# Kernel tuning notes

Measured on AMD Instinct MI355X. Metric: run time of the kernel, lower is better.

The kernel has to match this reference:

```python
import jax, jax.numpy as jnp
import numpy as np

PATCH = 3  # patch_size=3, stride=1
B, C, H, W = 8, 256, 64, 64


def _extract_patches(x):
    # x: (c, h, w) -> (c*PATCH*PATCH, N) with N = (h-2)*(w-2), valid 3x3 patches
    c, h, w = x.shape
    hh, ww = h - PATCH + 1, w - PATCH + 1
    pats = jnp.stack([x[:, i:i + hh, j:j + ww]
                      for i in range(PATCH) for j in range(PATCH)], axis=0)  # (9, c, hh, ww)
    return pats.reshape(PATCH * PATCH * c, hh * ww)


def _index_to_flow(max_idx):
    # max_idx: (hh, ww) int -> flow (h, w, 2) padded by 2 at bottom/right
    hh, ww = max_idx.shape
    flow_w = (max_idx % ww).astype(jnp.float32)
    flow_h = (max_idx // ww).astype(jnp.float32)
    gy, gx = jnp.meshgrid(jnp.arange(hh, dtype=jnp.float32),
                          jnp.arange(ww, dtype=jnp.float32), indexing='ij')
    flow = jnp.stack((flow_w - gx, flow_h - gy), axis=2)  # (hh, ww, 2)
    return jnp.pad(flow, ((0, 2), (0, 2), (0, 0)))


def _per_image(feat_in, feat_ref):
    c, h, w = feat_in.shape
    hh, ww = h - PATCH + 1, w - PATCH + 1
    # channel-wise L2 normalize each spatial position (F.normalize dim=0, eps=1e-12)
    feat_in = feat_in / jnp.maximum(jnp.linalg.norm(feat_in, axis=0, keepdims=True), 1e-12)
    feat_ref = feat_ref / jnp.maximum(jnp.linalg.norm(feat_ref, axis=0, keepdims=True), 1e-12)
    Pi = _extract_patches(feat_in)    # (k, N)
    Pr = _extract_patches(feat_ref)   # (k, N)
    # is_norm=True: normalize ref patches (norm + 1e-5, per BasicSR feature_match_index)
    Pr = Pr / (jnp.linalg.norm(Pr, axis=0, keepdims=True) + 1e-5)
    corr = Pi.T @ Pr                  # (N, N) exhaustive patch correlation
    max_val = corr.max(axis=1)
    max_idx = jnp.argmax(corr, axis=1)
    # norm_input=True: divide by input patch norms
    max_val = max_val / jnp.linalg.norm(Pi, axis=0)
    max_val = max_val.reshape(hh, ww)
    max_idx = max_idx.reshape(hh, ww)
    sim = jnp.pad(max_val, ((1, 1), (1, 1)))[None]  # (1, h, w)
    flow = _index_to_flow(max_idx)                   # (h, w, 2)
    # nine down-right shifts (fill 0 at top-left), tensor_shift semantics
    shifted = jnp.stack([jnp.pad(flow[:h - i, :w - j], ((i, 0), (j, 0), (0, 0)))
                         for i in range(3) for j in range(3)], axis=0)  # (9, h, w, 2)
    return flow, shifted, sim


def setup_inputs() -> dict:
    key = jax.random.key(0)
    k1, k2 = jax.random.split(key)
    features1 = jax.random.normal(k1, (B, C, H, W), dtype=jnp.float32)
    features2 = jax.random.normal(k2, (B, C, H, W), dtype=jnp.float32)
    return {"features1": features1, "features2": features2}


def reference(features1, features2):
    pre_flow, pre_offset, pre_similarity = jax.vmap(_per_image)(features1, features2)
    # pre_flow: (b,h,w,2); pre_offset: (b,9,h,w,2); pre_similarity: (b,1,h,w)
    return pre_flow, pre_offset, pre_similarity
```

## Files before the change

### kernel.cpp

```cpp
#include <hip/hip_runtime.h>

typedef unsigned short u16;
typedef unsigned char u8;
typedef unsigned int u32;
typedef __bf16 bf16x8 __attribute__((ext_vector_type(8)));
typedef float f32x4 __attribute__((ext_vector_type(4)));

constexpr int BATCH = 8;
constexpr int C = 256;
constexpr int H = 64;
constexpr int W = 64;
constexpr int HW = H * W;
constexpr int HH = 62, WW = 62;
constexpr int NQ = HH * WW;
constexpr int SEG = 8;
constexpr int NBLK_RED = 536;

constexpr size_t OFF_RNORM = 0;
constexpr size_t OFF_RESV = 262144;
constexpr size_t OFF_RESI = 385280;
constexpr size_t OFF_PV = 508416;
constexpr size_t OFF_PI = OFF_PV + 62980096;
constexpr size_t OFF_SLOT0 = OFF_PI + 15745024;
constexpr size_t SP_H1 = 0;
constexpr size_t SP_L1 = 2097152;
constexpr size_t SP_H2 = 4194304;
constexpr size_t SP_L2 = 6291456;
constexpr size_t SP_Q = 8388608;
constexpr size_t SLOT_BYTES = 75513856;
constexpr size_t PVIMG = (size_t)NQ * 512;

typedef const __attribute__((address_space(1))) unsigned int* gas_ptr;
typedef __attribute__((address_space(3))) unsigned int* las_ptr;
__device__ __forceinline__ void gl16(const void* g, void* l) {
  __builtin_amdgcn_global_load_lds((gas_ptr)g, (las_ptr)l, 16, 0, 0);
}

__device__ __forceinline__ int pre_of(int ki) {
  if (ki <= 62) return ki * (ki + 1) / 2;
  int r = 123 - ki;
  return 1953 + 1891 - r * (r + 1) / 2;
}

__global__ __launch_bounds__(256) void norm_kernel(const float* __restrict__ f1,
                                                   const float* __restrict__ f2,
                                                   float* __restrict__ rnorm) {
  int by = blockIdx.x;
  int tensor = blockIdx.y;
  const float* f = tensor ? f2 : f1;
  int b = by >> 6, y = by & 63;
  int x = threadIdx.x & 63;
  int cq = threadIdx.x >> 6;
  const float* base = f + ((size_t)b * C) * HW + y * W + x;
  float s = 0.f;
  for (int c = cq; c < C; c += 4) {
    float v = base[(size_t)c * HW];
    s = fmaf(v, v, s);
  }
  __shared__ float sm[4][64];
  sm[cq][x] = s;
  __syncthreads();
  if (threadIdx.x < 64) {
    float t = sm[0][x] + sm[1][x] + sm[2][x] + sm[3][x];
    float nrm = fmaxf(sqrtf(t), 1e-12f);
    rnorm[((size_t)tensor * BATCH + b) * HW + y * W + x] = 1.0f / nrm;
  }
}

__device__ __forceinline__ void convert_body(int chunk, int tensor, int bi,
                                             const float* __restrict__ f1,
                                             const float* __restrict__ f2,
                                             const float* __restrict__ rnorm,
                                             char* slot, char* smemraw, int t) {
  typedef u32 row_t[257];
  row_t* sm = (row_t*)smemraw;
  int pos0 = chunk * 32;
  const float* f = (tensor ? f2 : f1) + (size_t)bi * C * HW;
  const float* rn = rnorm + ((size_t)tensor * BATCH + bi) * HW + pos0;
  u16* dh = (u16*)(slot + (tensor ? SP_H2 : SP_H1)) + (size_t)pos0 * C;
  u16* dl = (u16*)(slot + (tensor ? SP_L2 : SP_L1)) + (size_t)pos0 * C;

  int px = t & 31, cg = t >> 5;
  float r = rn[px];
  for (int kk = 0; kk < 32; ++kk) {
    int c = (cg << 5) + kk;
    float v = f[(size_t)c * HW + pos0 + px] * r;
    __bf16 h = (__bf16)v;
    float hf = (float)h;
    __bf16 lo = (__bf16)(v - hf);
    sm[px][c] = ((u32)__builtin_bit_cast(u16, h) << 16) | (u32)__builtin_bit_cast(u16, lo);
  }
  __syncthreads();
  int px2 = t >> 3, seg = t & 7;
  int c0 = seg * 32;
  for (int g8 = 0; g8 < 4; ++g8) {
    u32 hw0, hw1, hw2, hw3, lw0, lw1, lw2, lw3;
    u32 a, b2;
    a = sm[px2][c0 + g8 * 8 + 0]; b2 = sm[px2][c0 + g8 * 8 + 1];
    hw0 = (a >> 16) | (b2 & 0xFFFF0000u); lw0 = (a & 0xFFFFu) | (b2 << 16);
    a = sm[px2][c0 + g8 * 8 + 2]; b2 = sm[px2][c0 + g8 * 8 + 3];
    hw1 = (a >> 16) | (b2 & 0xFFFF0000u); lw1 = (a & 0xFFFFu) | (b2 << 16);
    a = sm[px2][c0 + g8 * 8 + 4]; b2 = sm[px2][c0 + g8 * 8 + 5];
    hw2 = (a >> 16) | (b2 & 0xFFFF0000u); lw2 = (a & 0xFFFFu) | (b2 << 16);
    a = sm[px2][c0 + g8 * 8 + 6]; b2 = sm[px2][c0 + g8 * 8 + 7];
    hw3 = (a >> 16) | (b2 & 0xFFFF0000u); lw3 = (a & 0xFFFFu) | (b2 << 16);
    size_t off = (size_t)px2 * C + c0 + g8 * 8;
    uint4 hv; hv.x = hw0; hv.y = hw1; hv.z = hw2; hv.w = hw3;
    uint4 lv; lv.x = lw0; lv.y = lw1; lv.z = lw2; lv.w = lw3;
    *(uint4*)(dh + off) = hv;
    *(uint4*)(dl + off) = lv;
  }
}

__device__ __forceinline__ void pgemm_body(int bid, char* slot, char* smem, int t) {
  const u16* hi1 = (const u16*)(slot + SP_H1);
  const u16* lo1 = (const u16*)(slot + SP_L1);
  const u16* hi2 = (const u16*)(slot + SP_H2);
  const u16* lo2 = (const u16*)(slot + SP_L2);
  float* P = (float*)(slot + SP_Q);

  int swz = (bid & 7) * 128 + (bid >> 3);
  int p0 = (swz >> 5) << 7, q0 = (swz & 31) << 7;

  int l = t & 63, w = t >> 6, wm = w >> 1, wn = w & 1;
  int lr = l & 15, lh = l >> 4;

  const u16* srcs[4] = {hi1 + (size_t)p0 * 256, lo1 + (size_t)p0 * 256,
                        hi2 + (size_t)q0 * 256, lo2 + (size_t)q0 * 256};

  f32x4 acc[4][4];
#pragma unroll
  for (int mf = 0; mf < 4; ++mf)
#pragma unroll
    for (int nf = 0; nf < 4; ++nf)
      acc[mf][nf] = (f32x4){0.f, 0.f, 0.f, 0.f};

  auto stage = [&](int b, int kt) {
    char* base = smem + b * 32768;
#pragma unroll
    for (int pl = 0; pl < 4; ++pl) {
      const u16* s = srcs[pl];
#pragma unroll
      for (int wq = 0; wq < 2; ++wq) {
        int ci = (w * 2 + wq) * 64 + l;
        int row = ci >> 2, sl = ci & 3;
        int q = sl ^ ((row >> 1) & 3);
        size_t goff = (size_t)row * 256 + kt * 32 + (q << 3);
        gl16(s + goff, base + pl * 8192 + (w * 2 + wq) * 1024 + l * 16);
      }
    }
  };

  stage(0, 0);
  __syncthreads();

  for (int kt = 0; kt < 8; ++kt) {
    int b = kt & 1;
    if (kt < 7) stage(b ^ 1, kt + 1);
    char* sAh = smem + b * 32768;
    char* sAl = sAh + 8192;
    char* sBh = sAh + 16384;
    char* sBl = sAh + 24576;
    bf16x8 ah[4], al[4];
#pragma unroll
    for (int mf = 0; mf < 4; ++mf) {
      int row = wm * 64 + mf * 16 + lr;
      int off = row * 64 + ((lh ^ ((row >> 1) & 3)) << 4);
      ah[mf] = *(const bf16x8*)(sAh + off);
      al[mf] = *(const bf16x8*)(sAl + off);
    }
#pragma unroll
    for (int nf = 0; nf < 4; ++nf) {
      int row = wn * 64 + nf * 16 + lr;
      int off = row * 64 + ((lh ^ ((row >> 1) & 3)) << 4);
      bf16x8 bh = *(const bf16x8*)(sBh + off);
      bf16x8 bl = *(const bf16x8*)(sBl + off);
#pragma unroll
      for (int mf = 0; mf < 4; ++mf) {
        acc[mf][nf] = __builtin_amdgcn_mfma_f32_16x16x32_bf16(ah[mf], bh, acc[mf][nf], 0, 0, 0);
        acc[mf][nf] = __builtin_amdgcn_mfma_f32_16x16x32_bf16(al[mf], bh, acc[mf][nf], 0, 0, 0);
        acc[mf][nf] = __builtin_amdgcn_mfma_f32_16x16x32_bf16(ah[mf], bl, acc[mf][nf], 0, 0, 0);
      }
    }
    __syncthreads();
  }

  float* sq = (float*)smem;
#pragma unroll
  for (int pass = 0; pass < 2; ++pass) {
    if (pass) __syncthreads();
    if (wn == pass) {
      float* buf = sq + wm * 4352;
#pragma unroll
      for (int mf = 0; mf < 4; ++mf)
#pragma unroll
        for (int nf = 0; nf < 4; ++nf)
#pragma unroll
          for (int j = 0; j < 4; ++j)
            buf[(mf * 16 + lh * 4 + j) * 68 + nf * 16 + lr] = acc[mf][nf][j];
      *(f32x4*)(buf + l * 68 + 64) = (f32x4){0.f, 0.f, 0.f, 0.f};
    }
    __syncthreads();
    int tid2 = t & 127, sel = t >> 7;
    int ax = tid2 & 63, halfj = tid2 >> 6;
    const float* S = sq + sel * 4352;
    int rr1 = ax + 1 > 63 ? 63 : ax + 1;
    int rr2 = ax + 2 > 63 ? 63 : ax + 2;
    const float* S0 = S + ax * 68;
    const float* S1 = S + rr1 * 68;
    const float* S2 = S + rr2 * 68;
    int planeIdx = (((p0 >> 6) + sel) << 6) + (q0 >> 6) + pass;
    float* Qp = P + (((size_t)planeIdx) << 12);
#pragma unroll
    for (int gi = 0; gi < 4; ++gi) {
      int g = halfj * 4 + gi;
      int c0 = g * 8;
      float r0[12], r1a[12], r2a[12];
#pragma unroll
      for (int u = 0; u < 3; ++u) {
        *(f32x4*)(r0 + u * 4) = *(const f32x4*)(S0 + c0 + u * 4);
        *(f32x4*)(r1a + u * 4) = *(const f32x4*)(S1 + c0 + u * 4);
        *(f32x4*)(r2a + u * 4) = *(const f32x4*)(S2 + c0 + u * 4);
      }
      f32x4 qv0, qv1;
#pragma unroll
      for (int e = 0; e < 4; ++e) qv0[e] = r0[e] + r1a[e + 1] + r2a[e + 2];
#pragma unroll
      for (int e = 0; e < 4; ++e) qv1[e] = r0[e + 4] + r1a[e + 5] + r2a[e + 6];
      float* Qg = Qp + g * 512 + (ax << 2);
      *(f32x4*)(Qg) = qv0;
      *(f32x4*)(Qg + 256) = qv1;
    }
  }
}

__device__ __forceinline__ void reduce_body(int rid, const char* slot,
                                            float* pval8, u8* pidx8, int t) {
  const float* QT = (const float*)(slot + SP_Q);

  int bid = rid;
  int ki = 0;
  for (ki = 0; ki < 123; ++ki) {
    int d = ki - 61; if (d < 0) d = -d;
    int ns = (62 - d + SEG - 1) / SEG;
    if (bid < ns) break;
    bid -= ns;
  }
  int k = ki - 61;
  int ystart = k < 0 ? -k : 0;
  int yend = k > 0 ? 61 - k : 61;
  int y0 = ystart + bid * SEG;
  int y1 = y0 + SEG; if (y1 > yend + 1) y1 = yend + 1;
  int sid0 = pre_of(ki) + (y0 - ystart);
  int pmax = yend + 2;

  int w2 = t >> 6, l = t & 63;

  float A[16], B[16], P0[16], P1[16], P2[16];

  auto ld = [&](int p, float* D) {
    const float* gp = QT + (((size_t)((p << 6) + (p + k))) << 12) + (l << 2);
#pragma unroll
    for (int h = 0; h < 2; ++h) {
      const float* g2 = gp + ((w2 + h * 4) << 9);
      *(f32x4*)(D + h * 8) = *(const f32x4*)(g2);
      *(f32x4*)(D + h * 8 + 4) = *(const f32x4*)(g2 + 256);
    }
  };

  auto candstep = [&](int y, const float* D0, const float* D1, const float* D2) {
#pragma unroll
    for (int h = 0; h < 2; ++h) {
      int ww = w2 + h * 4;
      float best = __uint_as_float(0xFF800000u);
      int bbb = 0;
#pragma unroll
      for (int s = 0; s < 8; ++s) {
        float c = D0[h * 8 + s] + D1[h * 8 + s] + D2[h * 8 + s];
        bool valid = (ww * 8 + s) <= 61;
        if (valid && c > best) { best = c; bbb = s; }
      }
      size_t o = (size_t)(sid0 + (y - y0)) * 512 + (ww << 6) + l;
      pval8[o] = best;
      pidx8[o] = (u8)bbb;
    }
  };

  ld(y0, A);
  ld(y0 + 1, B);
  ld(y0 + 2, P0);
  ld(y0 + 3 > pmax ? pmax : y0 + 3, P1);
  ld(y0 + 4 > pmax ? pmax : y0 + 4, P2);

  int y = y0;
  while (true) {
    candstep(y, A, B, P0);
#pragma unroll
    for (int s = 0; s < 16; ++s) { A[s] = B[s]; B[s] = P0[s]; }
    if (++y >= y1) break;
    ld(y + 4 > pmax ? pmax : y + 4, P0);
    candstep(y, A, B, P1);
#pragma unroll
    for (int s = 0; s < 16; ++s) { A[s] = B[s]; B[s] = P1[s]; }
    if (++y >= y1) break;
    ld(y + 4 > pmax ? pmax : y + 4, P1);
    candstep(y, A, B, P2);
#pragma unroll
    for (int s = 0; s < 16; ++s) { A[s] = B[s]; B[s] = P2[s]; }
    if (++y >= y1) break;
    ld(y + 4 > pmax ? pmax : y + 4, P2);
  }
}

__global__ __launch_bounds__(256) void convert_kernel(const float* __restrict__ f1,
                                                      const float* __restrict__ f2,
                                                      const float* __restrict__ rnorm,
                                                      int bi, char* __restrict__ slot) {
  __shared__ __align__(16) char smem[33024];
  convert_body(blockIdx.x, blockIdx.y, bi, f1, f2, rnorm, slot, smem, threadIdx.x);
}

__global__ __launch_bounds__(256, 2) void merged_kernel(const float* __restrict__ f1,
                                                        const float* __restrict__ f2,
                                                        const float* __restrict__ rnorm,
                                                        char* __restrict__ ws,
                                                        int pg_img, int rd_img, int cv_img) {
  __shared__ __align__(16) char smem[65536];
  int bx = blockIdx.x, t = threadIdx.x;
  char* slot0 = ws + OFF_SLOT0;

  if (bx < 1608) {
    int m = bx % 3;
    if (m < 2) {
      int pid = (bx / 3) * 2 + m;
      if (pg_img >= 0 && pid < 1024)
        pgemm_body(pid, slot0 + (size_t)(pg_img & 1) * SLOT_BYTES, smem, t);
    } else {
      int rid = bx / 3;
      if (rd_img >= 0) {
        float* pv = (float*)(ws + OFF_PV) + (size_t)rd_img * PVIMG;
        u8* pi = (u8*)(ws + OFF_PI) + (size_t)rd_img * PVIMG;
        reduce_body(rid, slot0 + (size_t)(rd_img & 1) * SLOT_BYTES, pv, pi, t);
      }
    }
  } else {
    int cid = bx - 1608;
    if (cv_img >= 0)
      convert_body(cid & 127, cid >> 7, cv_img, f1, f2, rnorm,
                   slot0 + (size_t)(cv_img & 1) * SLOT_BYTES, smem, t);
  }
}

__global__ __launch_bounds__(256) void combine_kernel(const char* __restrict__ ws,
                                                      float* __restrict__ resv,
                                                      int* __restrict__ residx) {
  int q = blockIdx.x * 256 + threadIdx.x;
  if (q >= NQ) return;
  int b = blockIdx.y;
  const float* pval8 = (const float*)(ws + OFF_PV) + (size_t)b * PVIMG;
  const u8* pidx8 = (const u8*)(ws + OFF_PI) + (size_t)b * PVIMG;
  int y = q / 62, ax = q - y * 62;
  float best = __uint_as_float(0xFF800000u);
  int bjy = 0, bw = 0;
  for (int jy = 0; jy < 62; ++jy) {
    int ki = 61 + jy - y;
    int sid = pre_of(ki) + (y < jy ? y : jy);
    const float* p = pval8 + (size_t)sid * 512 + ax;
#pragma unroll
    for (int ww = 0; ww < 8; ++ww) {
      float v = p[ww << 6];
      if (v > best) { best = v; bjy = jy; bw = ww; }
    }
  }
  int kib = 61 + bjy - y;
  int sidb = pre_of(kib) + (y < bjy ? y : bjy);
  int bb = pidx8[(size_t)sidb * 512 + (bw << 6) + ax];
  resv[(size_t)b * NQ + q] = best;
  residx[(size_t)b * NQ + q] = bjy * 62 + bw * 8 + bb;
}

__global__ __launch_bounds__(256) void assemble_kernel(const float* __restrict__ res_val,
                                                       const int* __restrict__ res_idx,
                                                       float* __restrict__ out) {
  int gid = blockIdx.x * 256 + threadIdx.x;
  if (gid >= BATCH * HW) return;
  int b = gid >> 12;
  int y = (gid >> 6) & 63;
  int x = gid & 63;

  float* out_flow = out;
  float* out_off = out + (size_t)BATCH * HW * 2;
  float* out_sim = out + (size_t)BATCH * HW * 2 + (size_t)BATCH * 9 * HW * 2;

  auto flow_at = [&](int yy, int xx, float* fx, float* fy) {
    if (yy >= 0 && yy < HH && xx >= 0 && xx < WW) {
      int idx = res_idx[(size_t)b * NQ + yy * WW + xx];
      *fx = (float)(idx % WW - xx);
      *fy = (float)(idx / WW - yy);
    } else {
      *fx = 0.f;
      *fy = 0.f;
    }
  };

  float fx, fy;
  flow_at(y, x, &fx, &fy);
  size_t fo = ((size_t)b * HW + y * W + x) * 2;
  out_flow[fo + 0] = fx;
  out_flow[fo + 1] = fy;

#pragma unroll
  for (int sft = 0; sft < 9; ++sft) {
    int i = sft / 3, jj = sft % 3;
    float ox, oy;
    flow_at(y - i, x - jj, &ox, &oy);
    size_t o = (((size_t)b * 9 + sft) * HW + y * W + x) * 2;
    out_off[o + 0] = ox;
    out_off[o + 1] = oy;
  }

  float sim = 0.f;
  if (y >= 1 && y <= HH && x >= 1 && x <= WW) {
    float mv = res_val[(size_t)b * NQ + (y - 1) * WW + (x - 1)];
    sim = mv * (1.0f / ((3.0f + 1e-5f) * 3.0f));
  }
  out_sim[(size_t)b * HW + y * W + x] = sim;
}

extern "C" void kernel_launch(void* const* d_in, const int* in_sizes, int n_in,
                              void* d_out, int out_size, void* d_ws, size_t ws_size,
                              hipStream_t stream) {
  const float* f1 = (const float*)d_in[0];
  const float* f2 = (const float*)d_in[1];
  float* out = (float*)d_out;
  char* ws = (char*)d_ws;

  float* rnorm = (float*)(ws + OFF_RNORM);
  float* resv = (float*)(ws + OFF_RESV);
  int* residx = (int*)(ws + OFF_RESI);
  char* slot0 = ws + OFF_SLOT0;

  norm_kernel<<<dim3(BATCH * H, 2), 256, 0, stream>>>(f1, f2, rnorm);
  convert_kernel<<<dim3(128, 2), 256, 0, stream>>>(f1, f2, rnorm, 0, slot0);

  for (int i = 0; i < 8; ++i) {
    int cv = (i + 1 < 8) ? i + 1 : -1;
    merged_kernel<<<1864, 256, 0, stream>>>(f1, f2, rnorm, ws, i, i - 1, cv);
  }
  merged_kernel<<<1864, 256, 0, stream>>>(f1, f2, rnorm, ws, -1, 7, -1);

  combine_kernel<<<dim3(16, BATCH), 256, 0, stream>>>(ws, resv, residx);

  int total = BATCH * HW;
  assemble_kernel<<<(total + 255) / 256, 256, 0, stream>>>(resv, residx, out);
}
```

Before: 482.9 us.

## Single-buffer GEMM LDS and split epilogue to raise occupancy to four blocks

Removes the double-buffered shared-memory staging in the patch GEMM, so each k-step loads its tile and synchronises before computing. The epilogue that sums the 3x3 diagonals now runs in four passes, one 64x64 quadrant per wave, instead of two passes over two quadrants, so it fits in a single 33 KB buffer. Shared memory drops from 64 KB to about 33 KB and launch bounds go from 2 to 4 blocks per CU, aiming for more overlap through occupancy. In exchange, loads are no longer prefetched while the MFMAs run, there are more barriers per tile, and the register cap is tighter, which may cause spills.

```diff
diff --git a/kernel.cpp b/kernel.cpp
--- a/kernel.cpp
+++ b/kernel.cpp
@@ -135,8 +135,7 @@
     for (int nf = 0; nf < 4; ++nf)
       acc[mf][nf] = (f32x4){0.f, 0.f, 0.f, 0.f};
 
-  auto stage = [&](int b, int kt) {
-    char* base = smem + b * 32768;
+  auto stage = [&](int kt) {
 #pragma unroll
     for (int pl = 0; pl < 4; ++pl) {
       const u16* s = srcs[pl];
@@ -146,21 +145,18 @@
         int row = ci >> 2, sl = ci & 3;
         int q = sl ^ ((row >> 1) & 3);
         size_t goff = (size_t)row * 256 + kt * 32 + (q << 3);
-        gl16(s + goff, base + pl * 8192 + (w * 2 + wq) * 1024 + l * 16);
+        gl16(s + goff, smem + pl * 8192 + (w * 2 + wq) * 1024 + l * 16);
       }
     }
   };
 
-  stage(0, 0);
-  __syncthreads();
-
   for (int kt = 0; kt < 8; ++kt) {
-    int b = kt & 1;
-    if (kt < 7) stage(b ^ 1, kt + 1);
-    char* sAh = smem + b * 32768;
-    char* sAl = sAh + 8192;
-    char* sBh = sAh + 16384;
-    char* sBl = sAh + 24576;
+    stage(kt);
+    __syncthreads();
+    char* sAh = smem;
+    char* sAl = smem + 8192;
+    char* sBh = smem + 16384;
+    char* sBl = smem + 24576;
     bf16x8 ah[4], al[4];
 #pragma unroll
     for (int mf = 0; mf < 4; ++mf) {
@@ -187,33 +183,31 @@
 
   float* sq = (float*)smem;
 #pragma unroll
-  for (int pass = 0; pass < 2; ++pass) {
-    if (pass) __syncthreads();
-    if (wn == pass) {
-      float* buf = sq + wm * 4352;
+  for (int pp = 0; pp < 4; ++pp) {
+    int sel = pp >> 1, wnq = pp & 1;
+    if (pp) __syncthreads();
+    if (wm == sel && wn == wnq) {
 #pragma unroll
       for (int mf = 0; mf < 4; ++mf)
 #pragma unroll
         for (int nf = 0; nf < 4; ++nf)
 #pragma unroll
           for (int j = 0; j < 4; ++j)
-            buf[(mf * 16 + lh * 4 + j) * 68 + nf * 16 + lr] = acc[mf][nf][j];
-      *(f32x4*)(buf + l * 68 + 64) = (f32x4){0.f, 0.f, 0.f, 0.f};
+            sq[(mf * 16 + lh * 4 + j) * 68 + nf * 16 + lr] = acc[mf][nf][j];
+      *(f32x4*)(sq + l * 68 + 64) = (f32x4){0.f, 0.f, 0.f, 0.f};
     }
     __syncthreads();
-    int tid2 = t & 127, sel = t >> 7;
-    int ax = tid2 & 63, halfj = tid2 >> 6;
-    const float* S = sq + sel * 4352;
+    int ax = t & 63, halfj = (t >> 6) & 1, jg = t >> 7;
     int rr1 = ax + 1 > 63 ? 63 : ax + 1;
     int rr2 = ax + 2 > 63 ? 63 : ax + 2;
-    const float* S0 = S + ax * 68;
-    const float* S1 = S + rr1 * 68;
-    const float* S2 = S + rr2 * 68;
-    int planeIdx = (((p0 >> 6) + sel) << 6) + (q0 >> 6) + pass;
+    const float* S0 = sq + ax * 68;
+    const float* S1 = sq + rr1 * 68;
+    const float* S2 = sq + rr2 * 68;
+    int planeIdx = (((p0 >> 6) + sel) << 6) + (q0 >> 6) + wnq;
     float* Qp = P + (((size_t)planeIdx) << 12);
 #pragma unroll
-    for (int gi = 0; gi < 4; ++gi) {
-      int g = halfj * 4 + gi;
+    for (int gi = 0; gi < 2; ++gi) {
+      int g = halfj * 4 + jg * 2 + gi;
       int c0 = g * 8;
       float r0[12], r1a[12], r2a[12];
 #pragma unroll
@@ -320,12 +314,12 @@
   convert_body(blockIdx.x, blockIdx.y, bi, f1, f2, rnorm, slot, smem, threadIdx.x);
 }
 
-__global__ __launch_bounds__(256, 2) void merged_kernel(const float* __restrict__ f1,
+__global__ __launch_bounds__(256, 4) void merged_kernel(const float* __restrict__ f1,
                                                         const float* __restrict__ f2,
                                                         const float* __restrict__ rnorm,
                                                         char* __restrict__ ws,
                                                         int pg_img, int rd_img, int cv_img) {
-  __shared__ __align__(16) char smem[65536];
+  __shared__ __align__(16) char smem[33024];
   int bx = blockIdx.x, t = threadIdx.x;
   char* slot0 = ws + OFF_SLOT0;
 
```

New measurement: 576.1 us. 1.19x slower.
